# Optimization experiments

Hardware: AMD Instinct MI355X
Metric: run time of the kernel (lower is better)

The kernel has to match this reference:

```python
import jax, jax.numpy as jnp
import numpy as np
from jax import lax

EPS = 1e-8

def squash(x, axis=-1):
    # s = (|x|^2 / (1+|x|^2)) * x / |x|, norm over `axis`
    sq = jnp.sum(x * x, axis=axis, keepdims=True)
    return (sq / (1.0 + sq)) * x / jnp.sqrt(sq + EPS)

def _conv(x, w, b, stride):
    y = lax.conv_general_dilated(x, w, window_strides=(stride, stride), padding='VALID',
                                 dimension_numbers=('NCHW', 'OIHW', 'NCHW'))
    return y + b[None, :, None, None]

def setup_inputs() -> dict:
    key = jax.random.key(0)
    ks = jax.random.split(key, 12)
    B = 256
    return {
        'x': jax.random.uniform(ks[0], (B, 1, 28, 28), jnp.float32),
        'conv1_w': jax.random.normal(ks[1], (256, 1, 9, 9), jnp.float32) * 0.1,
        'conv1_b': jax.random.normal(ks[2], (256,), jnp.float32) * 0.01,
        'conv2_w': jax.random.normal(ks[3], (256, 256, 9, 9), jnp.float32) * 0.02,
        'conv2_b': jax.random.normal(ks[4], (256,), jnp.float32) * 0.01,
        'W': jax.random.normal(ks[5], (10, 1152, 8, 16), jnp.float32) * 0.05,
        'dec_w1': jax.random.normal(ks[6], (160, 512), jnp.float32) * 0.05,
        'dec_b1': jnp.zeros((512,), jnp.float32),
        'dec_w2': jax.random.normal(ks[7], (512, 1024), jnp.float32) * 0.04,
        'dec_b2': jnp.zeros((1024,), jnp.float32),
        'dec_w3': jax.random.normal(ks[8], (1024, 784), jnp.float32) * 0.03,
        'dec_b3': jnp.zeros((784,), jnp.float32),
    }

def reference(x, conv1_w, conv1_b, conv2_w, conv2_b, W, dec_w1, dec_b1, dec_w2, dec_b2, dec_w3, dec_b3):
    B = x.shape[0]
    h = jax.nn.relu(_conv(x, conv1_w, conv1_b, 1))          # [B,256,20,20]
    h = jax.nn.relu(_conv(h, conv2_w, conv2_b, 2))          # [B,256,6,6]
    u = squash(h.reshape(B, 1152, 8))                       # [B,1152,8]
    # u_hat[b,c,n,f] = sum_d u[b,n,d] * W[c,n,d,f]
    u_hat = jnp.einsum('bnd,cndf->bcnf', u, W)              # [B,10,1152,16]
    # dynamic routing, 3 iterations; softmax over the 1152 input-capsule axis
    # (faithful to original: softmax dim=2, b constant along the 16 axis)
    b_logits = jnp.zeros((B, 10, 1152), u_hat.dtype)
    v = None
    for i in range(3):
        c = jax.nn.softmax(b_logits, axis=2)                # [B,10,1152]
        s = jnp.einsum('bcn,bcnf->bcf', c, u_hat)           # [B,10,16]
        v = squash(s)
        if i != 2:
            b_logits = b_logits + jnp.einsum('bcf,bcnf->bcn', v, u_hat)
    class_probs = jnp.sqrt(jnp.sum(v * v, axis=-1) + EPS)   # [B,10]
    idx = jnp.argmax(class_probs, axis=-1)
    mask = jax.nn.one_hot(idx, 10, dtype=v.dtype)           # [B,10]
    r = (v * mask[:, :, None]).reshape(B, 160)
    r = jax.nn.relu(r @ dec_w1 + dec_b1)
    r = jax.nn.relu(r @ dec_w2 + dec_b2)
    recons = jax.nn.sigmoid(r @ dec_w3 + dec_b3)            # [B,784]
    return (class_probs, recons)
```

## Files before the change

kernel.cpp:

```cpp
#include <hip/hip_runtime.h>
#include <hip/hip_bf16.h>
#include <math.h>

typedef _Float16 f16;
typedef f16 f16x8 __attribute__((ext_vector_type(8)));
typedef f16 f16x4 __attribute__((ext_vector_type(4)));
typedef float f32x16 __attribute__((ext_vector_type(16)));


__global__ __launch_bounds__(256) void conv1_kernel(
    const float* __restrict__ x, const float* __restrict__ w,
    const float* __restrict__ bias, f16* __restrict__ outh,
    float* __restrict__ outf, int mode)
{
    const int b = blockIdx.y;
    const int cg = blockIdx.x;
    const int t = threadIdx.x;

    __shared__ float xs[784];
    __shared__ float wt[81 * 16];
    __shared__ float bs[16];

    for (int i = t; i < 784; i += 256) xs[i] = x[b * 784 + i];
    for (int i = t; i < 1296; i += 256) {
        int k = i >> 4, cc = i & 15;
        wt[i] = w[(cg * 16 + cc) * 81 + k];
    }
    if (t < 16) bs[t] = bias[cg * 16 + t];
    __syncthreads();

    if (t >= 200) return;
    const int pos = t * 2;
    const int oy = pos / 20, ox = pos % 20;
    float4 A0[4], A1[4];
    #pragma unroll
    for (int g = 0; g < 4; ++g) { A0[g] = make_float4(0,0,0,0); A1[g] = make_float4(0,0,0,0); }

    for (int ky = 0; ky < 9; ++ky) {
        const float* xr = &xs[(oy + ky) * 28 + ox];
        #pragma unroll
        for (int kx = 0; kx < 9; ++kx) {
            float x0 = xr[kx], x1 = xr[kx + 1];
            const float4* wp = (const float4*)&wt[(ky * 9 + kx) << 4];
            #pragma unroll
            for (int g = 0; g < 4; ++g) {
                float4 wv = wp[g];
                A0[g].x = fmaf(x0, wv.x, A0[g].x); A0[g].y = fmaf(x0, wv.y, A0[g].y);
                A0[g].z = fmaf(x0, wv.z, A0[g].z); A0[g].w = fmaf(x0, wv.w, A0[g].w);
                A1[g].x = fmaf(x1, wv.x, A1[g].x); A1[g].y = fmaf(x1, wv.y, A1[g].y);
                A1[g].z = fmaf(x1, wv.z, A1[g].z); A1[g].w = fmaf(x1, wv.w, A1[g].w);
            }
        }
    }

    float va[16], vb[16];
    #pragma unroll
    for (int g = 0; g < 4; ++g) {
        va[g*4+0] = fmaxf(A0[g].x + bs[g*4+0], 0.f);
        va[g*4+1] = fmaxf(A0[g].y + bs[g*4+1], 0.f);
        va[g*4+2] = fmaxf(A0[g].z + bs[g*4+2], 0.f);
        va[g*4+3] = fmaxf(A0[g].w + bs[g*4+3], 0.f);
        vb[g*4+0] = fmaxf(A1[g].x + bs[g*4+0], 0.f);
        vb[g*4+1] = fmaxf(A1[g].y + bs[g*4+1], 0.f);
        vb[g*4+2] = fmaxf(A1[g].z + bs[g*4+2], 0.f);
        vb[g*4+3] = fmaxf(A1[g].w + bs[g*4+3], 0.f);
    }

    if (mode == 0) {
        size_t base0 = ((size_t)b * 400 + pos) * 256 + cg * 16;
        f16x8 H;
        #pragma unroll
        for (int q = 0; q < 8; ++q) H[q] = (f16)va[q];
        *(f16x8*)(outh + base0) = H;
        #pragma unroll
        for (int q = 0; q < 8; ++q) H[q] = (f16)va[8+q];
        *(f16x8*)(outh + base0 + 8) = H;
        size_t base1 = base0 + 256;
        #pragma unroll
        for (int q = 0; q < 8; ++q) H[q] = (f16)vb[q];
        *(f16x8*)(outh + base1) = H;
        #pragma unroll
        for (int q = 0; q < 8; ++q) H[q] = (f16)vb[8+q];
        *(f16x8*)(outh + base1 + 8) = H;
    } else {
        #pragma unroll
        for (int q = 0; q < 16; ++q) {
            size_t base = (size_t)(b * 256 + cg * 16 + q) * 400 + pos;
            outf[base] = va[q]; outf[base + 1] = vb[q];
        }
    }
}

__global__ __launch_bounds__(256) void wprep_kernel(
    const float* __restrict__ w, f16* __restrict__ Wf,
    const float* __restrict__ W, f16* __restrict__ Wr)
{
    const int co = blockIdx.x, t = threadIdx.x;
    __shared__ float wl[20736];
    for (int i = t; i < 20736; i += 256) wl[i] = w[(size_t)co * 20736 + i];
    __syncthreads();
    for (int tap = 0; tap < 81; ++tap) {
        size_t o = ((size_t)tap * 256 + co) * 256 + t;
        Wf[o] = (f16)wl[t * 81 + tap];
    }
    const int base = co * 5760;
    for (int i = t; i < 5760; i += 256) Wr[base + i] = (f16)W[base + i];
}

#define GLOAD16(GSRC, LDST) \
    __builtin_amdgcn_global_load_lds( \
        (const __attribute__((address_space(1))) void*)(GSRC), \
        (__attribute__((address_space(3))) void*)(LDST), 16, 0, 0)

__global__ __launch_bounds__(256, 2) void conv2_async(
    const f16* __restrict__ A, const f16* __restrict__ B,
    float* __restrict__ partial, int nslice, int spk, int nwg)
{
    const int cpx = nwg >> 3;
    const int wg = (blockIdx.x & 7) * cpx + (blockIdx.x >> 3);
    const int mblk = wg / nslice;
    const int kslice = wg % nslice;

    const int t = threadIdx.x;
    const int lane = t & 63, w = t >> 6;
    const int wm = w >> 1, wn = w & 1;

    __shared__ f16 sA3[3][4096];
    __shared__ f16 sB3[3][8192];

    const f16* aBase[2];
    #pragma unroll
    for (int q = 0; q < 2; ++q) {
        int m = mblk * 128 + q * 64 + lane;
        int b_ = m / 36, s_ = m % 36;
        aBase[q] = A + b_ * 102400 + ((s_ / 6) * 40 + (s_ % 6) * 2) * 256 + w * 8;
    }
    const f16* bBase[4];
    #pragma unroll
    for (int q = 0; q < 4; ++q)
        bBase[q] = B + (q * 64 + lane) * 256 + w * 8;

    const int g0 = kslice * spk;
    const int len = min(spk, 648 - g0);

    auto issue = [&](int gstep, int buf) {
        const int tap = gstep >> 3;
        const int kc = (gstep & 7) << 5;
        const int ky = tap / 9, kx = tap - ky * 9;
        const int ao = (ky * 20 + kx) * 256 + kc;
        const int bo = tap * 65536 + kc;
        f16* la = &sA3[buf][w * 1024];
        f16* lb = &sB3[buf][w * 2048];
        GLOAD16(aBase[0] + ao, la);
        GLOAD16(aBase[1] + ao, la + 512);
        GLOAD16(bBase[0] + bo, lb);
        GLOAD16(bBase[1] + bo, lb + 512);
        GLOAD16(bBase[2] + bo, lb + 1024);
        GLOAD16(bBase[3] + bo, lb + 1536);
    };

    const int kh = lane >> 5;
    const int rArow = wm * 64 + (lane & 31);
    const int rBrow = wn * 128 + (lane & 31);
    int offA[2], offB[2];
    #pragma unroll
    for (int h = 0; h < 2; ++h) {
        offA[h] = ((h * 2 + kh) << 11) + rArow * 16;
        offB[h] = ((h * 2 + kh) << 12) + rBrow * 16;
    }

    f32x16 acc00 = {}, acc01 = {}, acc02 = {}, acc03 = {};
    f32x16 acc10 = {}, acc11 = {}, acc12 = {}, acc13 = {};

    issue(g0, 0);
    if (len > 1) issue(g0 + 1, 1);

    for (int s = 0; s < len; ++s) {
        const int buf = s % 3;
        if (s + 1 < len) { asm volatile("s_waitcnt vmcnt(6)" ::: "memory"); }
        else             { asm volatile("s_waitcnt vmcnt(0)" ::: "memory"); }
        __builtin_amdgcn_s_barrier();
        asm volatile("" ::: "memory");
        if (s + 2 < len) issue(g0 + s + 2, (s + 2) % 3);

        const char* baseA = (const char*)sA3 + buf * 8192;
        const char* baseB = (const char*)sB3 + buf * 16384;
        #pragma unroll
        for (int h = 0; h < 2; ++h) {
            f16x8 a0 = *(const f16x8*)(baseA + offA[h]);
            f16x8 a1 = *(const f16x8*)(baseA + offA[h] + 512);
            f16x8 b0 = *(const f16x8*)(baseB + offB[h]);
            f16x8 b1 = *(const f16x8*)(baseB + offB[h] + 512);
            f16x8 b2 = *(const f16x8*)(baseB + offB[h] + 1024);
            f16x8 b3 = *(const f16x8*)(baseB + offB[h] + 1536);
            acc00 = __builtin_amdgcn_mfma_f32_32x32x16_f16(a0, b0, acc00, 0, 0, 0);
            acc01 = __builtin_amdgcn_mfma_f32_32x32x16_f16(a0, b1, acc01, 0, 0, 0);
            acc02 = __builtin_amdgcn_mfma_f32_32x32x16_f16(a0, b2, acc02, 0, 0, 0);
            acc03 = __builtin_amdgcn_mfma_f32_32x32x16_f16(a0, b3, acc03, 0, 0, 0);
            acc10 = __builtin_amdgcn_mfma_f32_32x32x16_f16(a1, b0, acc10, 0, 0, 0);
            acc11 = __builtin_amdgcn_mfma_f32_32x32x16_f16(a1, b1, acc11, 0, 0, 0);
            acc12 = __builtin_amdgcn_mfma_f32_32x32x16_f16(a1, b2, acc12, 0, 0, 0);
            acc13 = __builtin_amdgcn_mfma_f32_32x32x16_f16(a1, b3, acc13, 0, 0, 0);
        }
    }

    float* pp = partial + (size_t)kslice * 2359296;
    const int colb = wn * 128 + (lane & 31);
    const int rowb = mblk * 128 + wm * 64 + 4 * (lane >> 5);
    #pragma unroll
    for (int a = 0; a < 2; ++a) {
        #pragma unroll
        for (int nf = 0; nf < 4; ++nf) {
            const f32x16 v = (a == 0)
                ? (nf == 0 ? acc00 : nf == 1 ? acc01 : nf == 2 ? acc02 : acc03)
                : (nf == 0 ? acc10 : nf == 1 ? acc11 : nf == 2 ? acc12 : acc13);
            const int col = colb + nf * 32;
            const int rb = rowb + a * 32;
            #pragma unroll
            for (int r = 0; r < 16; ++r) {
                int row = rb + (r & 3) + 8 * (r >> 2);
                pp[(size_t)row * 256 + col] = v[r];
            }
        }
    }
}

__global__ __launch_bounds__(256) void reduce_kernel(
    const float* __restrict__ partial, const float* __restrict__ bias,
    float* __restrict__ u, int ks)
{
    const int b = blockIdx.x, t = threadIdx.x;
    __shared__ float ld[36 * 260];
    const int cog = t & 63;
    const int srow = t >> 6;
    const float4 bv = *(const float4*)(bias + cog * 4);
    #pragma unroll
    for (int q = 0; q < 9; ++q) {
        const int s = srow + q * 4;
        const size_t idx = ((size_t)(b * 36 + s)) * 256 + cog * 4;
        float a0 = bv.x, a1 = bv.y, a2 = bv.z, a3 = bv.w;
        for (int k = 0; k < ks; ++k) {
            float4 p = *(const float4*)(partial + (size_t)k * 2359296 + idx);
            a0 += p.x; a1 += p.y; a2 += p.z; a3 += p.w;
        }
        float4 a = make_float4(fmaxf(a0, 0.f), fmaxf(a1, 0.f),
                               fmaxf(a2, 0.f), fmaxf(a3, 0.f));
        *(float4*)&ld[s * 260 + cog * 4] = a;
    }
    __syncthreads();
    for (int n = t; n < 1152; n += 256) {
        const int f0 = n * 8;
        float vals[8]; float sq = 0.f;
        int co = f0 / 36;
        int si = f0 - co * 36;
        #pragma unroll
        for (int d = 0; d < 8; ++d) {
            float v = ld[si * 260 + co];
            vals[d] = v; sq += v * v;
            if (++si == 36) { si = 0; ++co; }
        }
        float scale = (sq / (1.f + sq)) / sqrtf(sq + 1e-8f);
        #pragma unroll
        for (int d = 0; d < 8; ++d) u[(size_t)b * 9216 + f0 + d] = vals[d] * scale;
    }
}

#define C2_CHUNK 2
__global__ __launch_bounds__(384) void conv2_kernel(
    const float* __restrict__ in, const float* __restrict__ w,
    const float* __restrict__ bias, float* __restrict__ out)
{
    const int bg = blockIdx.y;
    const int ct = blockIdx.x;
    const int t = threadIdx.x;

    __shared__ float wl[C2_CHUNK][81][64];
    __shared__ float il[C2_CHUNK][4][20][24];

    const int cg = t & 15;
    const int slot = t >> 4;
    const int bb = slot / 6;
    const int oy = slot % 6;

    float4 acc[6];
    #pragma unroll
    for (int i = 0; i < 6; ++i) acc[i] = make_float4(0,0,0,0);

    for (int cc0 = 0; cc0 < 256; cc0 += C2_CHUNK) {
        for (int idx = t; idx < C2_CHUNK * 5184; idx += 384) {
            int ci = idx / 5184;
            int r = idx - ci * 5184;
            int kk = r >> 6;
            int co = r & 63;
            wl[ci][kk][co] = w[(size_t)(ct * 64 + co) * 20736 + (cc0 + ci) * 81 + kk];
        }
        for (int idx = t; idx < C2_CHUNK * 1600; idx += 384) {
            int ci = idx / 1600;
            int r = idx - ci * 1600;
            int bb2 = r / 400;
            int p = r - bb2 * 400;
            int y = p / 20;
            int xx = p - y * 20;
            il[ci][bb2][y][(xx & 1) * 12 + (xx >> 1)] =
                in[(size_t)((bg * 4 + bb2) * 256 + cc0 + ci) * 400 + p];
        }
        __syncthreads();

        #pragma unroll
        for (int ci = 0; ci < C2_CHUNK; ++ci) {
            for (int ky = 0; ky < 9; ++ky) {
                const int y = oy * 2 + ky;
                const float4* rowp = (const float4*)&il[ci][bb][y][0];
                float a[24];
                #pragma unroll
                for (int q = 0; q < 6; ++q) *(((float4*)a) + q) = rowp[q];
                #pragma unroll
                for (int kx = 0; kx < 9; ++kx) {
                    const int k = ky * 9 + kx;
                    float4 wv = *(const float4*)&wl[ci][k][cg * 4];
                    const int base = (kx & 1) ? (12 + (kx >> 1)) : (kx >> 1);
                    #pragma unroll
                    for (int ox = 0; ox < 6; ++ox) {
                        float av = a[base + ox];
                        acc[ox].x = fmaf(av, wv.x, acc[ox].x);
                        acc[ox].y = fmaf(av, wv.y, acc[ox].y);
                        acc[ox].z = fmaf(av, wv.z, acc[ox].z);
                        acc[ox].w = fmaf(av, wv.w, acc[ox].w);
                    }
                }
            }
        }
        __syncthreads();
    }

    const int b = bg * 4 + bb;
    const int c0 = ct * 64 + cg * 4;
    float4 bv = *(const float4*)&bias[c0];
    #pragma unroll
    for (int ox = 0; ox < 6; ++ox) {
        int sdx = oy * 6 + ox;
        size_t ob = (size_t)b * 9216 + sdx;
        out[ob + (size_t)(c0 + 0) * 36] = fmaxf(acc[ox].x + bv.x, 0.f);
        out[ob + (size_t)(c0 + 1) * 36] = fmaxf(acc[ox].y + bv.y, 0.f);
        out[ob + (size_t)(c0 + 2) * 36] = fmaxf(acc[ox].z + bv.z, 0.f);
        out[ob + (size_t)(c0 + 3) * 36] = fmaxf(acc[ox].w + bv.w, 0.f);
    }
}

__global__ __launch_bounds__(256) void squash_kernel(float* __restrict__ h)
{
    const int cap = blockIdx.x * 256 + threadIdx.x;
    float4* p = (float4*)(h + (size_t)cap * 8);
    float4 v0 = p[0], v1 = p[1];
    float sq = v0.x*v0.x + v0.y*v0.y + v0.z*v0.z + v0.w*v0.w
             + v1.x*v1.x + v1.y*v1.y + v1.z*v1.z + v1.w*v1.w;
    float scale = (sq / (1.f + sq)) / sqrtf(sq + 1e-8f);
    v0.x *= scale; v0.y *= scale; v0.z *= scale; v0.w *= scale;
    v1.x *= scale; v1.y *= scale; v1.z *= scale; v1.w *= scale;
    p[0] = v0; p[1] = v1;
}

__global__ __launch_bounds__(256) void routing_kernel(
    const float* __restrict__ u, const f16* __restrict__ Wr,
    float* __restrict__ cp_out, float* __restrict__ vbuf)
{
    const int wg = ((blockIdx.x & 7) * 160) + (blockIdx.x >> 3);
    const int c = wg >> 7;
    const int bp = wg & 127;
    const int b0 = bp * 2, b1 = b0 + 1;
    const int t = threadIdx.x;
    const int lane = t & 63, wid = t >> 6;

    __shared__ f16 uhh[2 * 1152 * 16];
    __shared__ f16 clh[2 * 1152];
    __shared__ float red[512];
    __shared__ float rtmp[16];
    __shared__ float vv[2][16];

    {
        const int fg = t & 1;
        const int ng = t >> 1;
        const f16* Wc = Wr + (size_t)c * 147456;
        const float* ub0 = u + (size_t)b0 * 9216;
        const float* ub1 = u + (size_t)b1 * 9216;
        for (int j = 0; j < 9; ++j) {
            const int n = ng + (j << 7);
            const f16* wn = Wc + n * 128 + fg * 8;
            float4 u00 = *(const float4*)(ub0 + n * 8);
            float4 u01 = *(const float4*)(ub0 + n * 8 + 4);
            float4 u10 = *(const float4*)(ub1 + n * 8);
            float4 u11 = *(const float4*)(ub1 + n * 8 + 4);
            float ud0[8] = {u00.x,u00.y,u00.z,u00.w,u01.x,u01.y,u01.z,u01.w};
            float ud1[8] = {u10.x,u10.y,u10.z,u10.w,u11.x,u11.y,u11.z,u11.w};
            float a0[8] = {0,0,0,0,0,0,0,0}, a1[8] = {0,0,0,0,0,0,0,0};
            #pragma unroll
            for (int d = 0; d < 8; ++d) {
                f16x8 w8 = *(const f16x8*)(wn + (d << 4));
                #pragma unroll
                for (int e = 0; e < 8; ++e) {
                    float wf = (float)w8[e];
                    a0[e] = fmaf(ud0[d], wf, a0[e]);
                    a1[e] = fmaf(ud1[d], wf, a1[e]);
                }
            }
            f16x8 h0, h1;
            #pragma unroll
            for (int e = 0; e < 8; ++e) { h0[e] = (f16)a0[e]; h1[e] = (f16)a1[e]; }
            *(f16x8*)&uhh[(n << 4) + (fg << 3)] = h0;
            *(f16x8*)&uhh[18432 + (n << 4) + (fg << 3)] = h1;
        }
    }
    __syncthreads();

    float blr0[5] = {0,0,0,0,0}, blr1[5] = {0,0,0,0,0};
    const int nown = (t < 128) ? 5 : 4;

    for (int it = 0; it < 3; ++it) {
        float m0 = -1e30f, m1 = -1e30f;
        #pragma unroll
        for (int k = 0; k < 5; ++k) if (k < nown) {
            m0 = fmaxf(m0, blr0[k]); m1 = fmaxf(m1, blr1[k]);
        }
        #pragma unroll
        for (int o = 32; o > 0; o >>= 1) {
            m0 = fmaxf(m0, __shfl_xor(m0, o));
            m1 = fmaxf(m1, __shfl_xor(m1, o));
        }
        if (lane == 0) { rtmp[wid] = m0; rtmp[4 + wid] = m1; }
        __syncthreads();
        m0 = fmaxf(fmaxf(rtmp[0], rtmp[1]), fmaxf(rtmp[2], rtmp[3]));
        m1 = fmaxf(fmaxf(rtmp[4], rtmp[5]), fmaxf(rtmp[6], rtmp[7]));

        float s0 = 0.f, s1 = 0.f;
        #pragma unroll
        for (int k = 0; k < 5; ++k) if (k < nown) {
            float e0 = __expf(blr0[k] - m0);
            float e1 = __expf(blr1[k] - m1);
            clh[t + (k << 8)] = (f16)e0;
            clh[1152 + t + (k << 8)] = (f16)e1;
            s0 += e0; s1 += e1;
        }
        #pragma unroll
        for (int o = 32; o > 0; o >>= 1) {
            s0 += __shfl_xor(s0, o);
            s1 += __shfl_xor(s1, o);
        }
        if (lane == 0) { rtmp[8 + wid] = s0; rtmp[12 + wid] = s1; }
        __syncthreads();
        const float inv0 = 1.f / (rtmp[8] + rtmp[9] + rtmp[10] + rtmp[11]);
        const float inv1 = 1.f / (rtmp[12] + rtmp[13] + rtmp[14] + rtmp[15]);

        const int f = t & 15, g = t >> 4;
        float sa0 = 0.f, sa1 = 0.f;
        for (int n = g; n < 1152; n += 16) {
            sa0 = fmaf((float)clh[n], (float)uhh[(n << 4) + f], sa0);
            sa1 = fmaf((float)clh[1152 + n], (float)uhh[18432 + (n << 4) + f], sa1);
        }
        red[(g << 4) + f] = sa0;
        red[256 + (g << 4) + f] = sa1;
        __syncthreads();
        if (t < 32) {
            const int s = t >> 4;
            const int ff = t & 15;
            float sv = 0.f;
            #pragma unroll
            for (int gg = 0; gg < 16; ++gg) sv += red[s * 256 + (gg << 4) + ff];
            sv *= (s == 0) ? inv0 : inv1;
            float sq = sv * sv;
            #pragma unroll
            for (int o = 8; o > 0; o >>= 1) sq += __shfl_xor(sq, o);
            float scale = (sq / (1.f + sq)) / sqrtf(sq + 1e-8f);
            vv[s][ff] = sv * scale;
        }
        __syncthreads();

        if (it < 2) {
            float v0[16], v1[16];
            #pragma unroll
            for (int e = 0; e < 16; ++e) { v0[e] = vv[0][e]; v1[e] = vv[1][e]; }
            #pragma unroll
            for (int k = 0; k < 5; ++k) if (k < nown) {
                const int n = t + (k << 8);
                f16x8 q0 = *(const f16x8*)&uhh[n << 4];
                f16x8 q1 = *(const f16x8*)&uhh[(n << 4) + 8];
                f16x8 r0 = *(const f16x8*)&uhh[18432 + (n << 4)];
                f16x8 r1 = *(const f16x8*)&uhh[18432 + (n << 4) + 8];
                float d0 = 0.f, d1 = 0.f;
                #pragma unroll
                for (int e = 0; e < 8; ++e) {
                    d0 = fmaf((float)q0[e], v0[e], d0);
                    d0 = fmaf((float)q1[e], v0[8 + e], d0);
                    d1 = fmaf((float)r0[e], v1[e], d1);
                    d1 = fmaf((float)r1[e], v1[8 + e], d1);
                }
                blr0[k] += d0; blr1[k] += d1;
            }
        }
    }

    if (t < 32) {
        const int s = t >> 4;
        const int ff = t & 15;
        float v_ = vv[s][ff];
        float s2 = v_ * v_;
        #pragma unroll
        for (int o = 8; o > 0; o >>= 1) s2 += __shfl_xor(s2, o);
        const int b = (s == 0) ? b0 : b1;
        if (ff == 0) cp_out[b * 10 + c] = sqrtf(s2 + 1e-8f);
        vbuf[((b * 10 + c) << 4) + ff] = v_;
    }
}

__global__ __launch_bounds__(256) void dec12_kernel(
    const float* __restrict__ cp, const float* __restrict__ vbuf,
    const float* __restrict__ W1, const float* __restrict__ B1,
    const float* __restrict__ W2, const float* __restrict__ B2,
    float* __restrict__ h2)
{
    const int ot = blockIdx.x, bt = blockIdx.y, t = threadIdx.x;
    __shared__ float h1s[16][516];
    __shared__ float r16s[16][16];
    __shared__ int idxs[16];

    if (t < 16) {
        const int b = bt * 16 + t;
        float best = cp[b * 10];
        int idx = 0;
        #pragma unroll
        for (int cc = 1; cc < 10; ++cc) {
            float p = cp[b * 10 + cc];
            if (p > best) { best = p; idx = cc; }
        }
        idxs[t] = idx;
    }
    __syncthreads();
    {
        const int bb = t >> 4, f = t & 15;
        const int b = bt * 16 + bb;
        r16s[bb][f] = vbuf[((b * 10 + idxs[bb]) << 4) + f];
    }
    __syncthreads();

    {
        const int bb = t >> 4, tg = t & 15;
        const float* w = W1 + (size_t)idxs[bb] * 8192;
        float r[16];
        #pragma unroll
        for (int k = 0; k < 16; ++k) r[k] = r16s[bb][k];
        for (int j = tg; j < 512; j += 16) {
            float a = B1[j];
            #pragma unroll
            for (int k = 0; k < 16; ++k) a = fmaf(r[k], w[k * 512 + j], a);
            h1s[bb][j] = fmaxf(a, 0.f);
        }
    }
    __syncthreads();

    {
        const int bb = t >> 4;
        const int o = ot * 64 + (t & 15) * 4;
        float4 bv = *(const float4*)(B2 + o);
        float a0 = bv.x, a1 = bv.y, a2 = bv.z, a3 = bv.w;
        #pragma unroll 4
        for (int k = 0; k < 512; ++k) {
            float hv = h1s[bb][k];
            float4 w0 = *(const float4*)(W2 + (size_t)k * 1024 + o);
            a0 = fmaf(hv, w0.x, a0); a1 = fmaf(hv, w0.y, a1);
            a2 = fmaf(hv, w0.z, a2); a3 = fmaf(hv, w0.w, a3);
        }
        float* hw = h2 + (size_t)(bt * 16 + bb) * 1024 + o;
        hw[0] = fmaxf(a0, 0.f); hw[1] = fmaxf(a1, 0.f);
        hw[2] = fmaxf(a2, 0.f); hw[3] = fmaxf(a3, 0.f);
    }
}

__global__ __launch_bounds__(256) void dec3_kernel(
    const float* __restrict__ h2, const float* __restrict__ W3,
    const float* __restrict__ B3, float* __restrict__ out)
{
    const int ot = blockIdx.x, bt = blockIdx.y, t = threadIdx.x;
    const int bb = bt * 8 + (t >> 5);
    const int o = ot * 64 + (t & 31) * 2;
    if (o >= 784) return;

    float a0 = B3[o], a1 = B3[o + 1];
    const float* hr = h2 + (size_t)bb * 1024;
    #pragma unroll 4
    for (int k = 0; k < 1024; ++k) {
        float hv = hr[k];
        const float* wp = W3 + (size_t)k * 784 + o;
        a0 = fmaf(hv, wp[0], a0);
        a1 = fmaf(hv, wp[1], a1);
    }
    float* ow = out + (size_t)bb * 784 + o;
    ow[0] = 1.f / (1.f + expf(-a0));
    ow[1] = 1.f / (1.f + expf(-a1));
}

extern "C" void kernel_launch(void* const* d_in, const int* in_sizes, int n_in,
                              void* d_out, int out_size, void* d_ws, size_t ws_size,
                              hipStream_t stream) {
    const float* x   = (const float*)d_in[0];
    const float* w1  = (const float*)d_in[1];
    const float* b1  = (const float*)d_in[2];
    const float* w2  = (const float*)d_in[3];
    const float* b2  = (const float*)d_in[4];
    const float* W   = (const float*)d_in[5];
    const float* dw1 = (const float*)d_in[6];
    const float* db1 = (const float*)d_in[7];
    const float* dw2 = (const float*)d_in[8];
    const float* db2 = (const float*)d_in[9];
    const float* dw3 = (const float*)d_in[10];
    const float* db3 = (const float*)d_in[11];

    float* ws   = (float*)d_ws;
    float* outp = (float*)d_out;

    const size_t avail = ws_size / 4;
    int ks = 0;
    if      (avail >= 16498688ull + 7*2359296ull + 40960ull) ks = 7;
    else if (avail >= 16498688ull + 6*2359296ull + 40960ull) ks = 6;
    else if (avail >= 16498688ull + 4*2359296ull + 40960ull) ks = 4;
    else if (avail >= 16498688ull + 2*2359296ull + 40960ull) ks = 2;
    else if (avail >= 16498688ull + 1*2359296ull + 40960ull) ks = 1;

    if (ks > 0) {
        f16* Af = (f16*)ws;
        f16* Wf = (f16*)(ws + 13107200);
        f16* Wr = (f16*)(ws + 15761408);
        float* partial = ws + 16498688;
        float* vbuf = ws + 16498688 + (size_t)ks * 2359296;
        float* u  = ws;
        float* h2 = ws + 13107200;

        const int nwg = 72 * ks;
        const int spk = (648 + ks - 1) / ks;
        conv1_kernel<<<dim3(16, 256), 256, 0, stream>>>(x, w1, b1, Af, nullptr, 0);
        wprep_kernel<<<256, 256, 0, stream>>>(w2, Wf, W, Wr);
        conv2_async<<<nwg, 256, 0, stream>>>(Af, Wf, partial, ks, spk, nwg);
        reduce_kernel<<<256, 256, 0, stream>>>(partial, b2, u, ks);
        routing_kernel<<<1280, 256, 0, stream>>>(u, Wr, outp, vbuf);
        dec12_kernel<<<dim3(16, 16), 256, 0, stream>>>(outp, vbuf, dw1, db1, dw2, db2, h2);
        dec3_kernel<<<dim3(13, 32), 256, 0, stream>>>(h2, dw3, db3, outp + 2560);
    } else {
        float* c1   = ws;
        float* c2   = c1 + 26214400;
        float* vbuf = c2 + 2359296;
        float* h2   = vbuf + 40960;
        f16* Wr     = (f16*)(h2 + 262144);
        conv1_kernel<<<dim3(16, 256), 256, 0, stream>>>(x, w1, b1, nullptr, c1, 1);
        wprep_kernel<<<256, 256, 0, stream>>>(w2, (f16*)(h2 + 262144 + 368640), W, Wr);
        conv2_kernel<<<dim3(4, 64), 384, 0, stream>>>(c1, w2, b2, c2);
        squash_kernel<<<1152, 256, 0, stream>>>(c2);
        routing_kernel<<<1280, 256, 0, stream>>>(c2, Wr, outp, vbuf);
        dec12_kernel<<<dim3(16, 16), 256, 0, stream>>>(outp, vbuf, dw1, db1, dw2, db2, h2);
        dec3_kernel<<<dim3(13, 32), 256, 0, stream>>>(h2, dw3, db3, outp + 2560);
    }
}
```

Baseline: 453.2 us.

## Fold weight prep into conv1 launch and widen reduce blocks

The separate wprep kernel is merged into conv1 as an extra column of blocks (blockIdx.x==16). Those blocks transpose and convert the conv2 and routing weights to f16 alongside the conv1 work, which removes one launch and lets the two jobs run concurrently. The prep blocks now stage the weights through a smaller 64-channel chunked LDS buffer instead of an 81 KB one, which should raise occupancy. The reduce kernel moves to 512 threads per block for more parallelism in the partial-sum reduction, at the cost of some idle lanes in the row loop.

```diff
diff --git a/kernel.cpp b/kernel.cpp
--- a/kernel.cpp
+++ b/kernel.cpp
@@ -11,15 +11,36 @@
 __global__ __launch_bounds__(256) void conv1_kernel(
     const float* __restrict__ x, const float* __restrict__ w,
     const float* __restrict__ bias, f16* __restrict__ outh,
-    float* __restrict__ outf, int mode)
-{
+    float* __restrict__ outf, int mode,
+    const float* __restrict__ w2, f16* __restrict__ Wf,
+    const float* __restrict__ W, f16* __restrict__ Wr)
+{
+    __shared__ float smem[5184];
+    const int t = threadIdx.x;
+
+    if (blockIdx.x == 16) {
+        const int co = blockIdx.y;
+        for (int chunk = 0; chunk < 4; ++chunk) {
+            const int ci0 = chunk * 64;
+            for (int i = t; i < 5184; i += 256)
+                smem[i] = w2[(size_t)co * 20736 + ci0 * 81 + i];
+            __syncthreads();
+            const int ci = t & 63;
+            for (int tap = t >> 6; tap < 81; tap += 4)
+                Wf[((size_t)tap * 256 + co) * 256 + ci0 + ci] =
+                    (f16)smem[ci * 81 + tap];
+            __syncthreads();
+        }
+        const int base = co * 5760;
+        for (int i = t; i < 5760; i += 256) Wr[base + i] = (f16)W[base + i];
+        return;
+    }
+
+    float* xs = smem;
+    float* wt = smem + 784;
+    float* bs = smem + 2080;
     const int b = blockIdx.y;
     const int cg = blockIdx.x;
-    const int t = threadIdx.x;
-
-    __shared__ float xs[784];
-    __shared__ float wt[81 * 16];
-    __shared__ float bs[16];
 
     for (int i = t; i < 784; i += 256) xs[i] = x[b * 784 + i];
     for (int i = t; i < 1296; i += 256) {
@@ -89,22 +110,6 @@
             outf[base] = va[q]; outf[base + 1] = vb[q];
         }
     }
-}
-
-__global__ __launch_bounds__(256) void wprep_kernel(
-    const float* __restrict__ w, f16* __restrict__ Wf,
-    const float* __restrict__ W, f16* __restrict__ Wr)
-{
-    const int co = blockIdx.x, t = threadIdx.x;
-    __shared__ float wl[20736];
-    for (int i = t; i < 20736; i += 256) wl[i] = w[(size_t)co * 20736 + i];
-    __syncthreads();
-    for (int tap = 0; tap < 81; ++tap) {
-        size_t o = ((size_t)tap * 256 + co) * 256 + t;
-        Wf[o] = (f16)wl[t * 81 + tap];
-    }
-    const int base = co * 5760;
-    for (int i = t; i < 5760; i += 256) Wr[base + i] = (f16)W[base + i];
 }
 
 #define GLOAD16(GSRC, LDST) \
@@ -225,7 +230,7 @@
     }
 }
 
-__global__ __launch_bounds__(256) void reduce_kernel(
+__global__ __launch_bounds__(512) void reduce_kernel(
     const float* __restrict__ partial, const float* __restrict__ bias,
     float* __restrict__ u, int ks)
 {
@@ -235,20 +240,22 @@
     const int srow = t >> 6;
     const float4 bv = *(const float4*)(bias + cog * 4);
     #pragma unroll
-    for (int q = 0; q < 9; ++q) {
-        const int s = srow + q * 4;
-        const size_t idx = ((size_t)(b * 36 + s)) * 256 + cog * 4;
-        float a0 = bv.x, a1 = bv.y, a2 = bv.z, a3 = bv.w;
-        for (int k = 0; k < ks; ++k) {
-            float4 p = *(const float4*)(partial + (size_t)k * 2359296 + idx);
-            a0 += p.x; a1 += p.y; a2 += p.z; a3 += p.w;
-        }
-        float4 a = make_float4(fmaxf(a0, 0.f), fmaxf(a1, 0.f),
-                               fmaxf(a2, 0.f), fmaxf(a3, 0.f));
-        *(float4*)&ld[s * 260 + cog * 4] = a;
+    for (int q = 0; q < 5; ++q) {
+        const int s = srow + q * 8;
+        if (s < 36) {
+            const size_t idx = ((size_t)(b * 36 + s)) * 256 + cog * 4;
+            float a0 = bv.x, a1 = bv.y, a2 = bv.z, a3 = bv.w;
+            for (int k = 0; k < ks; ++k) {
+                float4 p = *(const float4*)(partial + (size_t)k * 2359296 + idx);
+                a0 += p.x; a1 += p.y; a2 += p.z; a3 += p.w;
+            }
+            float4 a = make_float4(fmaxf(a0, 0.f), fmaxf(a1, 0.f),
+                                   fmaxf(a2, 0.f), fmaxf(a3, 0.f));
+            *(float4*)&ld[s * 260 + cog * 4] = a;
+        }
     }
     __syncthreads();
-    for (int n = t; n < 1152; n += 256) {
+    for (int n = t; n < 1152; n += 512) {
         const int f0 = n * 8;
         float vals[8]; float sq = 0.f;
         int co = f0 / 36;
@@ -635,10 +642,10 @@
 
         const int nwg = 72 * ks;
         const int spk = (648 + ks - 1) / ks;
-        conv1_kernel<<<dim3(16, 256), 256, 0, stream>>>(x, w1, b1, Af, nullptr, 0);
-        wprep_kernel<<<256, 256, 0, stream>>>(w2, Wf, W, Wr);
+        conv1_kernel<<<dim3(17, 256), 256, 0, stream>>>(x, w1, b1, Af, nullptr, 0,
+                                                        w2, Wf, W, Wr);
         conv2_async<<<nwg, 256, 0, stream>>>(Af, Wf, partial, ks, spk, nwg);
-        reduce_kernel<<<256, 256, 0, stream>>>(partial, b2, u, ks);
+        reduce_kernel<<<256, 512, 0, stream>>>(partial, b2, u, ks);
         routing_kernel<<<1280, 256, 0, stream>>>(u, Wr, outp, vbuf);
         dec12_kernel<<<dim3(16, 16), 256, 0, stream>>>(outp, vbuf, dw1, db1, dw2, db2, h2);
         dec3_kernel<<<dim3(13, 32), 256, 0, stream>>>(h2, dw3, db3, outp + 2560);
@@ -648,8 +655,9 @@
         float* vbuf = c2 + 2359296;
         float* h2   = vbuf + 40960;
         f16* Wr     = (f16*)(h2 + 262144);
-        conv1_kernel<<<dim3(16, 256), 256, 0, stream>>>(x, w1, b1, nullptr, c1, 1);
-        wprep_kernel<<<256, 256, 0, stream>>>(w2, (f16*)(h2 + 262144 + 368640), W, Wr);
+        f16* Wfscr  = (f16*)(h2 + 262144 + 368640);
+        conv1_kernel<<<dim3(17, 256), 256, 0, stream>>>(x, w1, b1, nullptr, c1, 1,
+                                                        w2, Wfscr, W, Wr);
         conv2_kernel<<<dim3(4, 64), 384, 0, stream>>>(c1, w2, b2, c2);
         squash_kernel<<<1152, 256, 0, stream>>>(c2);
         routing_kernel<<<1280, 256, 0, stream>>>(c2, Wr, outp, vbuf);
```

After: 440.1 us (median of 2 runs). 2.9% less time.
